# Performance work log

Measured on AMD Instinct MI355X. Metric: run time of the kernel, lower is better.

The kernel has to match this reference:

```python
import jax, jax.numpy as jnp
import numpy as np

D_MODEL = 5120
N_HEADS = 8
D_HEAD = D_MODEL // N_HEADS          # 640
D_ROPE = 16
SPLIT_DIM = D_HEAD - D_ROPE          # 624
D_KV = 128
BATCH, SEQ = 2, 2048
ROPE_SCALE = 40.0


def _rope_cos_sin(seq_len):
    # inv_freq length = D_ROPE//4 (quirk of the original code)
    inv_freq = 1.0 / (10000.0 ** (jnp.arange(0, D_ROPE // 2, 2, dtype=jnp.float32) / (D_ROPE // 2)))
    t = jnp.arange(seq_len, dtype=jnp.float32) / ROPE_SCALE
    freqs = t[:, None] * inv_freq[None, :]            # [S, D_ROPE//4]
    emb = jnp.concatenate([freqs, freqs], axis=-1)    # [S, D_ROPE//2]
    cos = jnp.cos(emb)[None, :, None, :]              # [1,S,1,D_ROPE//2]
    sin = jnp.sin(emb)[None, :, None, :]
    return cos, sin


def _rotate_half(x):
    x1, x2 = jnp.split(x, 2, axis=-1)
    return jnp.concatenate([-x2, x1], axis=-1)


def _apply_rotary(x, cos, sin):
    r = cos.shape[-1]
    x_rot, x_base = x[..., :r], x[..., r:]
    x_rot = x_rot * cos + _rotate_half(x_rot) * sin
    return jnp.concatenate([x_rot, x_base], axis=-1)


def setup_inputs():
    key = jax.random.key(0)
    ks = jax.random.split(key, 18)
    s = 0.02
    inp = {
        'h': jax.random.normal(ks[0], (BATCH, SEQ, D_MODEL), dtype=jnp.float32),
        'W_dkv': jax.random.normal(ks[1], (D_MODEL, D_KV), dtype=jnp.float32) * s,
        'b_dkv': jnp.zeros((D_KV,), jnp.float32),
        'W_dq': jax.random.normal(ks[2], (D_MODEL, D_KV), dtype=jnp.float32) * s,
        'b_dq': jnp.zeros((D_KV,), jnp.float32),
        'W_uk': jax.random.normal(ks[3], (D_KV, N_HEADS * SPLIT_DIM), dtype=jnp.float32) * s,
        'b_uk': jnp.zeros((N_HEADS * SPLIT_DIM,), jnp.float32),
        'W_uv': jax.random.normal(ks[4], (D_KV, N_HEADS * D_HEAD), dtype=jnp.float32) * s,
        'b_uv': jnp.zeros((N_HEADS * D_HEAD,), jnp.float32),
        'W_uq': jax.random.normal(ks[5], (D_KV, N_HEADS * SPLIT_DIM), dtype=jnp.float32) * s,
        'b_uq': jnp.zeros((N_HEADS * SPLIT_DIM,), jnp.float32),
        'W_qr': jax.random.normal(ks[6], (D_KV, N_HEADS * D_ROPE), dtype=jnp.float32) * s,
        'b_qr': jnp.zeros((N_HEADS * D_ROPE,), jnp.float32),
        'W_kr': jax.random.normal(ks[7], (D_MODEL, N_HEADS * D_ROPE), dtype=jnp.float32) * s,
        'b_kr': jnp.zeros((N_HEADS * D_ROPE,), jnp.float32),
        'W_o': jax.random.normal(ks[8], (N_HEADS * D_HEAD, D_MODEL), dtype=jnp.float32) * s,
        'b_o': jnp.zeros((D_MODEL,), jnp.float32),
    }
    return inp


def reference(h, W_dkv, b_dkv, W_dq, b_dq, W_uk, b_uk, W_uv, b_uv,
              W_uq, b_uq, W_qr, b_qr, W_kr, b_kr, W_o, b_o):
    B, S, _ = h.shape
    c_kv = h @ W_dkv + b_dkv                                   # [B,S,D_KV]
    k = (c_kv @ W_uk + b_uk).reshape(B, S, N_HEADS, SPLIT_DIM)
    v = (c_kv @ W_uv + b_uv).reshape(B, S, N_HEADS, D_HEAD)
    c_q = h @ W_dq + b_dq
    q_base = (c_q @ W_uq + b_uq).reshape(B, S, N_HEADS, SPLIT_DIM)
    q_rot = (c_q @ W_qr + b_qr).reshape(B, S, N_HEADS, D_ROPE)
    cos, sin = _rope_cos_sin(S)
    q_rot = _apply_rotary(q_rot, cos, sin)
    k_rot = _apply_rotary((h @ W_kr + b_kr).reshape(B, S, N_HEADS, D_ROPE), cos, sin)
    q = jnp.concatenate([q_base, q_rot], axis=-1)              # [B,S,H,D_HEAD]
    k = jnp.concatenate([k, k_rot], axis=-1)                   # [B,S,H,D_HEAD]
    scores = jnp.einsum('bqhd,bkhd->bhqk', q, k) / jnp.sqrt(jnp.float32(D_HEAD))
    attn = jax.nn.softmax(scores, axis=-1)
    out = jnp.einsum('bhqk,bkhd->bqhd', attn, v)               # [B,S,H,D_HEAD]
    return out.reshape(B, S, N_HEADS * D_HEAD) @ W_o + b_o
```

## Files before the change

### kernel.cpp

```cpp
#include <hip/hip_runtime.h>


typedef unsigned short ushort_t;
typedef __attribute__((ext_vector_type(8)))  short          short8;
typedef __attribute__((ext_vector_type(8)))  unsigned short us8;
typedef __attribute__((ext_vector_type(4)))  float          f32x4;

#define SCALE_ATT 0.0395284707521047f

static __device__ inline unsigned short f2bf(float f) {
  union { float f; unsigned u; } v; v.f = f;
  unsigned r = (v.u + 0x7fffu + ((v.u >> 16) & 1u)) >> 16;
  return (unsigned short)r;
}
static __device__ inline float bf2f(unsigned short u) {
  union { unsigned u; float f; } v; v.u = ((unsigned)u) << 16;
  return v.f;
}
static __device__ inline unsigned cvt_pk_bf16(float a, float b) {
  unsigned r;
  asm("v_cvt_pk_bf16_f32 %0, %1, %2" : "=v"(r) : "v"(a), "v"(b));
  return r;
}
static __device__ inline f32x4 MFMA(short8 a, short8 b, f32x4 c) {
  return __builtin_amdgcn_mfma_f32_16x16x32_bf16(a, b, c, 0, 0, 0);
}

__global__ __launch_bounds__(256) void k_bvec_init(const float* __restrict__ bo,
                                                   float* __restrict__ bvec) {
  int n = blockIdx.x * 256 + threadIdx.x;
  bvec[n] = bo[n];
}

__global__ __launch_bounds__(128) void k_bqabs(const float* __restrict__ buq,
                                               const float* __restrict__ Wuk,
                                               float* __restrict__ bqabs) {
  int h = blockIdx.x, j = threadIdx.x;
  float acc = 0.f;
  const float* bq = buq + h * 624;
  const float* wk = Wuk + (size_t)j * 4992 + h * 624;
  for (int d = 0; d < 624; ++d) acc += bq[d] * wk[d];
  bqabs[h * 128 + j] = acc;
}

__global__ __launch_bounds__(256) void k_wqk(const float* __restrict__ Wuq,
                                             const float* __restrict__ Wuk,
                                             ushort_t* __restrict__ wqkT) {
  __shared__ float Aq[16 * 132];
  __shared__ float Ak[16 * 132];
  int jt = blockIdx.x, it = blockIdx.y, h = blockIdx.z;
  int i0 = it * 16, j0 = jt * 16;
  int t = threadIdx.x;
  int srow = t >> 4, sc0 = (t & 15) * 8;
  int ti = t & 15, tj = t >> 4;
  float acc = 0.f;
  for (int dc = 0; dc < 624; dc += 128) {
#pragma unroll
    for (int i = 0; i < 8; ++i) {
      int d = dc + sc0 + i;
      Aq[srow * 132 + sc0 + i] = (d < 624) ? Wuq[(size_t)(i0 + srow) * 4992 + h * 624 + d] : 0.f;
      Ak[srow * 132 + sc0 + i] = (d < 624) ? Wuk[(size_t)(j0 + srow) * 4992 + h * 624 + d] : 0.f;
    }
    __syncthreads();
    int cs = (624 - dc) < 128 ? (624 - dc) : 128;
    for (int d = 0; d < cs; d += 4) {
      const f32x4 a4 = *(const f32x4*)&Aq[ti * 132 + d];
      const f32x4 b4 = *(const f32x4*)&Ak[tj * 132 + d];
      acc += a4[0] * b4[0] + a4[1] * b4[1] + a4[2] * b4[2] + a4[3] * b4[3];
    }
    __syncthreads();
  }
  wqkT[(size_t)h * 16384 + (size_t)(j0 + tj) * 128 + (i0 + ti)] = f2bf(acc);
}

__global__ __launch_bounds__(256) void k_gemm1_sk(
    const float* __restrict__ H, const float* __restrict__ Wdkv,
    const float* __restrict__ Wdq, const float* __restrict__ Wkr,
    float* __restrict__ part) {
  __shared__ __align__(16) ushort_t As[64 * 72];
  __shared__ __align__(16) ushort_t Bs[192 * 72];
  const int tid = threadIdx.x;
  const int m0 = blockIdx.x * 64;
  const int n0 = blockIdx.y * 192;
  const int kc0 = blockIdx.z * 1280;
  const int lane = tid & 63, wid = tid >> 6;
  const int quad = lane >> 4, l15 = lane & 15;
  f32x4 acc[4][3];
#pragma unroll
  for (int a = 0; a < 4; ++a)
#pragma unroll
    for (int b = 0; b < 3; ++b) acc[a][b] = (f32x4){0.f, 0.f, 0.f, 0.f};
  const int ar = tid >> 2, ak0 = (tid & 3) * 16;
  const int br = tid >> 2, bsg = tid & 3;
  const int bkidx = br ^ (bsg << 4);
  const float* harow = H + (size_t)(m0 + ar) * 5120 + ak0;
  for (int kb = kc0; kb < kc0 + 1280; kb += 64) {
    const float* ap = harow + kb;
    us8 av0, av1;
#pragma unroll
    for (int i = 0; i < 8; ++i) { av0[i] = f2bf(ap[i]); av1[i] = f2bf(ap[8 + i]); }
    *(us8*)&As[ar * 72 + ak0] = av0;
    *(us8*)&As[ar * 72 + ak0 + 8] = av1;
#pragma unroll
    for (int g16 = 0; g16 < 3; ++g16) {
      const int lcol = g16 * 64 + bsg * 16;
      const int col = n0 + lcol;
      const float* base = (col < 128 ? Wdkv + col
                         : col < 256 ? Wdq + (col - 128)
                                     : Wkr + (col - 256)) + (size_t)(kb + br) * 128;
#pragma unroll
      for (int i = 0; i < 16; ++i)
        Bs[(lcol + i) * 72 + bkidx] = f2bf(base[i]);
    }
    __syncthreads();
#pragma unroll
    for (int ks = 0; ks < 2; ++ks) {
      short8 a[4], b[3];
#pragma unroll
      for (int mt = 0; mt < 4; ++mt)
        a[mt] = *(const short8*)&As[(mt * 16 + l15) * 72 + ks * 32 + quad * 8];
#pragma unroll
      for (int nt = 0; nt < 3; ++nt)
        b[nt] = *(const short8*)&Bs[(wid * 48 + nt * 16 + l15) * 72 +
                                    ((ks * 32 + quad * 8) ^ (((wid * 3 + nt) & 3) << 4))];
#pragma unroll
      for (int mt = 0; mt < 4; ++mt)
#pragma unroll
        for (int nt = 0; nt < 3; ++nt) acc[mt][nt] = MFMA(a[mt], b[nt], acc[mt][nt]);
    }
    __syncthreads();
  }
  const size_t pb = (size_t)blockIdx.z * 4096 * 384;
#pragma unroll
  for (int mt = 0; mt < 4; ++mt)
#pragma unroll
    for (int nt = 0; nt < 3; ++nt) {
      const int col = n0 + wid * 48 + nt * 16 + l15;
#pragma unroll
      for (int r = 0; r < 4; ++r) {
        const int row = m0 + mt * 16 + quad * 4 + r;
        part[pb + (size_t)row * 384 + col] = acc[mt][nt][r];
      }
    }
}

__global__ __launch_bounds__(384) void k_reduce(
    const float* __restrict__ part, const float* __restrict__ bdkv,
    const float* __restrict__ bdq, const float* __restrict__ bkr,
    ushort_t* __restrict__ ckv, ushort_t* __restrict__ cq,
    ushort_t* __restrict__ krot) {
  const int row = blockIdx.x;
  const int c = threadIdx.x;
  float v = 0.f;
#pragma unroll
  for (int ks = 0; ks < 4; ++ks)
    v += part[((size_t)ks * 4096 + row) * 384 + c];
  if (c < 128) {
    v += bdkv[c];
    ckv[(size_t)row * 128 + c] = f2bf(v);
  } else if (c < 256) {
    v += bdq[c - 128];
    cq[(size_t)row * 128 + (c - 128)] = f2bf(v);
  } else {
    v += bkr[c - 256];
    float partner = __shfl_xor(v, 4);
    const int j = (c - 256) & 15;
    const int head = (c - 256) >> 4;
    const int s = row & 2047, bb = row >> 11;
    const int j4 = j & 3;
    const float fr = (j4 == 0) ? 1.f : (j4 == 1) ? 0.1f : (j4 == 2) ? 0.01f : 0.001f;
    float sth, cth;
    __sincosf(s * 0.025f * fr, &sth, &cth);
    const float y = (j < 4) ? (v * cth - partner * sth)
                  : (j < 8) ? (v * cth + partner * sth) : v;
    krot[((size_t)((bb << 3) + head) * 2048 + s) * 16 + j] = f2bf(y);
  }
}

__global__ __launch_bounds__(256) void k_ckvt(const ushort_t* __restrict__ ckv,
                                              ushort_t* __restrict__ ckvT) {
  __shared__ __align__(16) ushort_t T[128 * 72];
  const int tid = threadIdx.x;
  const int s0 = blockIdx.x * 64;
  const int bb = s0 >> 11, sl = s0 & 2047;
  const int sr = tid >> 2, sseg = tid & 3;
  {
    const ushort_t* kp = ckv + ((size_t)s0 + sr) * 128 + sseg * 32;
    us8 v[4];
#pragma unroll
    for (int w = 0; w < 4; ++w) v[w] = *(const us8*)(kp + w * 8);
#pragma unroll
    for (int w = 0; w < 4; ++w)
#pragma unroll
      for (int i = 0; i < 8; ++i)
        T[(sseg * 32 + w * 8 + i) * 72 + sr] = v[w][i];
  }
  __syncthreads();
  const int vrow = tid >> 1, vk0 = (tid & 1) * 32;
#pragma unroll
  for (int w = 0; w < 4; ++w) {
    us8 t = *(const us8*)&T[vrow * 72 + vk0 + w * 8];
    *(us8*)(ckvT + ((size_t)bb * 128 + vrow) * 2048 + sl + vk0 + w * 8) = t;
  }
}

__global__ __launch_bounds__(256) void k_qrot(const ushort_t* __restrict__ cq,
                                              const float* __restrict__ Wqr,
                                              const float* __restrict__ bqr,
                                              ushort_t* __restrict__ qrot) {
  int gidx = blockIdx.x * 256 + threadIdx.x;
  int s = gidx & 2047, bh = gidx >> 11;
  int hh = bh & 7, bb = bh >> 3;
  const ushort_t* crow = cq + ((size_t)bb * 2048 + s) * 128;
  float acc[16];
#pragma unroll
  for (int j = 0; j < 16; ++j) acc[j] = bqr[hh * 16 + j];
  for (int k0 = 0; k0 < 128; k0 += 8) {
    us8 cv8 = *(const us8*)(crow + k0);
#pragma unroll
    for (int i = 0; i < 8; ++i) {
      float cv = bf2f(cv8[i]);
      const float* wr = Wqr + (size_t)(k0 + i) * 128 + hh * 16;
#pragma unroll
      for (int j = 0; j < 16; ++j) acc[j] += cv * wr[j];
    }
  }
  float y[16];
#pragma unroll
  for (int j4 = 0; j4 < 4; ++j4) {
    float fr = (j4 == 0) ? 1.f : (j4 == 1) ? 0.1f : (j4 == 2) ? 0.01f : 0.001f;
    float sth, cth;
    __sincosf(s * 0.025f * fr, &sth, &cth);
    y[j4] = acc[j4] * cth - acc[j4 + 4] * sth;
    y[j4 + 4] = acc[j4 + 4] * cth + acc[j4] * sth;
  }
#pragma unroll
  for (int j = 8; j < 16; ++j) y[j] = acc[j];
  us8 o0, o1;
#pragma unroll
  for (int j = 0; j < 8; ++j) {
    o0[j] = f2bf(y[j] * SCALE_ATT);
    o1[j] = f2bf(y[8 + j] * SCALE_ATT);
  }
  *(us8*)(qrot + (size_t)gidx * 16) = o0;
  *(us8*)(qrot + (size_t)gidx * 16 + 8) = o1;
}

__global__ __launch_bounds__(256) void k_qabs(const ushort_t* __restrict__ cq,
                                              const ushort_t* __restrict__ wqkT,
                                              const float* __restrict__ bqabs,
                                              ushort_t* __restrict__ qabs) {
  __shared__ __align__(16) ushort_t As[128 * 72];
  __shared__ __align__(16) ushort_t Bs[128 * 72];
  const int tid = threadIdx.x;
  const int m0 = blockIdx.x * 128, hh = blockIdx.y;
  const int lane = tid & 63, wid = tid >> 6;
  const int quad = lane >> 4, l15 = lane & 15;
  const int wm = wid & 1, wn = wid >> 1;
  f32x4 acc[4][4];
#pragma unroll
  for (int a = 0; a < 4; ++a)
#pragma unroll
    for (int b = 0; b < 4; ++b) acc[a][b] = (f32x4){0.f, 0.f, 0.f, 0.f};
  const int ar = tid >> 1, as0 = (tid & 1) * 32;
  for (int kb = 0; kb < 128; kb += 64) {
    const ushort_t* ap = cq + (size_t)(m0 + ar) * 128 + kb + as0;
    const ushort_t* bp = wqkT + (size_t)hh * 16384 + (size_t)ar * 128 + kb + as0;
#pragma unroll
    for (int w = 0; w < 4; ++w) {
      *(us8*)&As[ar * 72 + as0 + w * 8] = *(const us8*)(ap + w * 8);
      *(us8*)&Bs[ar * 72 + as0 + w * 8] = *(const us8*)(bp + w * 8);
    }
    __syncthreads();
#pragma unroll
    for (int ks = 0; ks < 2; ++ks) {
      short8 a[4], b[4];
#pragma unroll
      for (int mt = 0; mt < 4; ++mt)
        a[mt] = *(const short8*)&As[(wm * 64 + mt * 16 + l15) * 72 + ks * 32 + quad * 8];
#pragma unroll
      for (int nt = 0; nt < 4; ++nt)
        b[nt] = *(const short8*)&Bs[(wn * 64 + nt * 16 + l15) * 72 + ks * 32 + quad * 8];
#pragma unroll
      for (int mt = 0; mt < 4; ++mt)
#pragma unroll
        for (int nt = 0; nt < 4; ++nt) acc[mt][nt] = MFMA(a[mt], b[nt], acc[mt][nt]);
    }
    __syncthreads();
  }
#pragma unroll
  for (int mt = 0; mt < 4; ++mt)
#pragma unroll
    for (int nt = 0; nt < 4; ++nt) {
      int col = wn * 64 + nt * 16 + l15;
      float bias = bqabs[hh * 128 + col];
#pragma unroll
      for (int r = 0; r < 4; ++r) {
        int m = m0 + wm * 64 + mt * 16 + quad * 4 + r;
        int bb = m >> 11, s = m & 2047;
        qabs[((size_t)((bb << 3) + hh) * 2048 + s) * 128 + col] =
            f2bf((acc[mt][nt][r] + bias) * SCALE_ATT);
      }
    }
}

__global__ __launch_bounds__(256) void k_comb(const float* __restrict__ Wo,
                                              const float* __restrict__ Wuv,
                                              const float* __restrict__ buv,
                                              ushort_t* __restrict__ wcombT,
                                              float* __restrict__ bvec) {
  __shared__ __align__(16) ushort_t As[128 * 72];
  __shared__ __align__(16) ushort_t Bs[128 * 72];
  const int tid = threadIdx.x;
  const int n0 = blockIdx.x * 128, hh = blockIdx.y;
  const int lane = tid & 63, wid = tid >> 6;
  const int quad = lane >> 4, l15 = lane & 15;
  const int wm = wid & 1, wn = wid >> 1;
  f32x4 acc[4][4];
#pragma unroll
  for (int a = 0; a < 4; ++a)
#pragma unroll
    for (int b = 0; b < 4; ++b) acc[a][b] = (f32x4){0.f, 0.f, 0.f, 0.f};
  const int ad = tid >> 2, asg = tid & 3;
  const int an0 = asg * 32;
  const int akidx = ad ^ (asg << 4);
  const int bc = tid >> 1, bd0 = (tid & 1) * 32;
  const int bvc = tid >> 1, bvh = tid & 1;
  const int bsgr = (bvc >> 5) & 3;
  const float* buvh = buv + hh * 640;
  float bacc = 0.f;
  for (int kb = 0; kb < 640; kb += 64) {
    const float* ap = Wo + (size_t)(hh * 640 + kb + ad) * 5120 + n0 + an0;
#pragma unroll
    for (int i = 0; i < 32; ++i) As[(an0 + i) * 72 + akidx] = f2bf(ap[i]);
    const float* bp = Wuv + (size_t)bc * 5120 + hh * 640 + kb + bd0;
    us8 bv0, bv1, bv2, bv3;
#pragma unroll
    for (int i = 0; i < 8; ++i) {
      bv0[i] = f2bf(bp[i]); bv1[i] = f2bf(bp[8 + i]);
      bv2[i] = f2bf(bp[16 + i]); bv3[i] = f2bf(bp[24 + i]);
    }
    *(us8*)&Bs[bc * 72 + bd0] = bv0;
    *(us8*)&Bs[bc * 72 + bd0 + 8] = bv1;
    *(us8*)&Bs[bc * 72 + bd0 + 16] = bv2;
    *(us8*)&Bs[bc * 72 + bd0 + 24] = bv3;
    __syncthreads();
#pragma unroll
    for (int d8 = 0; d8 < 4; ++d8) {
      const int k0 = bvh * 32 + d8 * 8;
      const us8 a8 = *(const us8*)&As[bvc * 72 + (k0 ^ (bsgr << 4))];
      const f32x4 b4a = *(const f32x4*)&buvh[kb + k0];
      const f32x4 b4b = *(const f32x4*)&buvh[kb + k0 + 4];
      bacc += b4a[0] * bf2f(a8[0]) + b4a[1] * bf2f(a8[1]) +
              b4a[2] * bf2f(a8[2]) + b4a[3] * bf2f(a8[3]) +
              b4b[0] * bf2f(a8[4]) + b4b[1] * bf2f(a8[5]) +
              b4b[2] * bf2f(a8[6]) + b4b[3] * bf2f(a8[7]);
    }
#pragma unroll
    for (int ks = 0; ks < 2; ++ks) {
      short8 a[4], b[4];
#pragma unroll
      for (int mt = 0; mt < 4; ++mt)
        a[mt] = *(const short8*)&As[(wm * 64 + mt * 16 + l15) * 72 +
                                    ((ks * 32 + quad * 8) ^ (((wm * 2 + (mt >> 1)) & 3) << 4))];
#pragma unroll
      for (int nt = 0; nt < 4; ++nt)
        b[nt] = *(const short8*)&Bs[(wn * 64 + nt * 16 + l15) * 72 + ks * 32 + quad * 8];
#pragma unroll
      for (int mt = 0; mt < 4; ++mt)
#pragma unroll
        for (int nt = 0; nt < 4; ++nt) acc[mt][nt] = MFMA(a[mt], b[nt], acc[mt][nt]);
    }
    __syncthreads();
  }
#pragma unroll
  for (int mt = 0; mt < 4; ++mt)
#pragma unroll
    for (int nt = 0; nt < 4; ++nt) {
      int col = wn * 64 + nt * 16 + l15;
#pragma unroll
      for (int r = 0; r < 4; ++r) {
        int n = n0 + wm * 64 + mt * 16 + quad * 4 + r;
        wcombT[(size_t)n * 1024 + hh * 128 + col] = f2bf(acc[mt][nt][r]);
      }
    }
  atomicAdd(&bvec[n0 + bvc], bacc);
}

__global__ __launch_bounds__(256) void k_attn(const ushort_t* __restrict__ qabs,
                                              const ushort_t* __restrict__ qrot,
                                              const ushort_t* __restrict__ ckv,
                                              const ushort_t* __restrict__ krot,
                                              const ushort_t* __restrict__ ckvT,
                                              ushort_t* __restrict__ ctx) {
  __shared__ __align__(16) ushort_t Qs[64 * 168];
  __shared__ __align__(16) ushort_t Ks[64 * 168];
  __shared__ __align__(16) ushort_t Vt[128 * 72];
  __shared__ __align__(16) ushort_t Ps[64 * 72];
  const int tid = threadIdx.x;
  const int bh = blockIdx.y, bb = bh >> 3, hh = bh & 7;
  const int q0 = blockIdx.x * 64;
  const int lane = tid & 63, wid = tid >> 6;
  const int quad = lane >> 4, l15 = lane & 15;
  const int sr = tid >> 2, sseg = tid & 3;
  const int vrow = tid >> 1, vk0 = (tid & 1) * 32;
  (void)hh;
  {
    const ushort_t* qa = qabs + ((size_t)bh * 2048 + q0 + sr) * 128 + sseg * 32;
#pragma unroll
    for (int w = 0; w < 4; ++w)
      *(us8*)&Qs[sr * 168 + sseg * 32 + w * 8] = *(const us8*)(qa + w * 8);
    if (sseg == 0) {
      const ushort_t* qr = qrot + ((size_t)bh * 2048 + q0 + sr) * 16;
      *(us8*)&Qs[sr * 168 + 128] = *(const us8*)qr;
      *(us8*)&Qs[sr * 168 + 136] = *(const us8*)(qr + 8);
    }
    if (sseg == 1) {
      us8 z = (us8)0;
      *(us8*)&Qs[sr * 168 + 144] = z;
      *(us8*)&Qs[sr * 168 + 152] = z;
      *(us8*)&Ks[sr * 168 + 144] = z;
      *(us8*)&Ks[sr * 168 + 152] = z;
    }
  }
  us8 kreg[4], vreg[4], krr0, krr1;
  auto loadKV = [&](int key0) {
    const ushort_t* kp = ckv + ((size_t)bb * 2048 + key0 + sr) * 128 + sseg * 32;
#pragma unroll
    for (int w = 0; w < 4; ++w) kreg[w] = *(const us8*)(kp + w * 8);
    const ushort_t* vp = ckvT + ((size_t)bb * 128 + vrow) * 2048 + key0 + vk0;
#pragma unroll
    for (int w = 0; w < 4; ++w) vreg[w] = *(const us8*)(vp + w * 8);
    if (sseg == 0) {
      const ushort_t* kr = krot + ((size_t)bh * 2048 + key0 + sr) * 16;
      krr0 = *(const us8*)kr;
      krr1 = *(const us8*)(kr + 8);
    }
  };
  loadKV(0);
  f32x4 oacc[8];
#pragma unroll
  for (int i = 0; i < 8; ++i) oacc[i] = (f32x4){0.f, 0.f, 0.f, 0.f};
  float mrow[4] = {-1e30f, -1e30f, -1e30f, -1e30f};
  float lrow[4] = {0.f, 0.f, 0.f, 0.f};

  for (int kt = 0; kt < 32; ++kt) {
#pragma unroll
    for (int w = 0; w < 4; ++w)
      *(us8*)&Ks[sr * 168 + sseg * 32 + w * 8] = kreg[w];
    if (sseg == 0) {
      *(us8*)&Ks[sr * 168 + 128] = krr0;
      *(us8*)&Ks[sr * 168 + 136] = krr1;
    }
#pragma unroll
    for (int w = 0; w < 4; ++w)
      *(us8*)&Vt[vrow * 72 + vk0 + w * 8] = vreg[w];
    __syncthreads();
    f32x4 sacc[4];
#pragma unroll
    for (int nt = 0; nt < 4; ++nt) sacc[nt] = (f32x4){0.f, 0.f, 0.f, 0.f};
#pragma unroll
    for (int ks = 0; ks < 5; ++ks) {
      short8 aq = *(const short8*)&Qs[(wid * 16 + l15) * 168 + ks * 32 + quad * 8];
#pragma unroll
      for (int nt = 0; nt < 4; ++nt) {
        short8 bk = *(const short8*)&Ks[(nt * 16 + l15) * 168 + ks * 32 + quad * 8];
        sacc[nt] = MFMA(aq, bk, sacc[nt]);
      }
    }
    if (kt < 31) loadKV((kt + 1) * 64);
    float p[4][4];
#pragma unroll
    for (int r = 0; r < 4; ++r) {
      float mx = fmaxf(fmaxf(sacc[0][r], sacc[1][r]), fmaxf(sacc[2][r], sacc[3][r]));
#pragma unroll
      for (int off = 1; off < 16; off <<= 1) mx = fmaxf(mx, __shfl_xor(mx, off));
      if (mx > mrow[r]) {
        float alpha = __expf(mrow[r] - mx);
        mrow[r] = mx;
        lrow[r] *= alpha;
#pragma unroll
        for (int t8 = 0; t8 < 8; ++t8) oacc[t8][r] *= alpha;
      }
      float rs = 0.f;
#pragma unroll
      for (int nt = 0; nt < 4; ++nt) {
        float pv = __expf(sacc[nt][r] - mrow[r]);
        p[nt][r] = pv;
        rs += pv;
      }
      lrow[r] += rs;
    }
#pragma unroll
    for (int nt = 0; nt < 4; ++nt)
#pragma unroll
      for (int rp = 0; rp < 2; ++rp) {
        unsigned pk = cvt_pk_bf16(p[nt][2 * rp], p[nt][2 * rp + 1]);
        int ad = (wid * 16 + quad * 4 + 2 * rp) * 72 + nt * 16 + l15;
        Ps[ad] = (ushort_t)pk;
        Ps[ad + 72] = (ushort_t)(pk >> 16);
      }
    __syncthreads();
#pragma unroll
    for (int kk = 0; kk < 2; ++kk) {
      short8 pa = *(const short8*)&Ps[(wid * 16 + l15) * 72 + kk * 32 + quad * 8];
#pragma unroll
      for (int nt = 0; nt < 8; ++nt) {
        short8 vb = *(const short8*)&Vt[(nt * 16 + l15) * 72 + kk * 32 + quad * 8];
        oacc[nt] = MFMA(pa, vb, oacc[nt]);
      }
    }
    __syncthreads();
  }
#pragma unroll
  for (int r = 0; r < 4; ++r) {
#pragma unroll
    for (int off = 1; off < 16; off <<= 1) lrow[r] += __shfl_xor(lrow[r], off);
    float rl = 1.f / lrow[r];
    int row = q0 + wid * 16 + quad * 4 + r;
    size_t base = ((size_t)bb * 2048 + row) * 1024 + hh * 128;
#pragma unroll
    for (int nt = 0; nt < 8; ++nt)
      ctx[base + nt * 16 + l15] = f2bf(oacc[nt][r] * rl);
  }
}

__global__ __launch_bounds__(256) void k_final(const ushort_t* __restrict__ ctx,
                                               const ushort_t* __restrict__ wcombT,
                                               const float* __restrict__ bvec,
                                               float* __restrict__ out) {
  __shared__ __align__(16) ushort_t As[128 * 72];
  __shared__ __align__(16) ushort_t Bs[128 * 72];
  const int tid = threadIdx.x;
  const int m0 = blockIdx.x * 128, n0 = blockIdx.y * 128;
  const int lane = tid & 63, wid = tid >> 6;
  const int quad = lane >> 4, l15 = lane & 15;
  const int wm = wid & 1, wn = wid >> 1;
  f32x4 acc[4][4];
#pragma unroll
  for (int a = 0; a < 4; ++a)
#pragma unroll
    for (int b = 0; b < 4; ++b) acc[a][b] = (f32x4){0.f, 0.f, 0.f, 0.f};
  const int ar = tid >> 1, as0 = (tid & 1) * 32;
  const ushort_t* ap = ctx + (size_t)(m0 + ar) * 1024 + as0;
  const ushort_t* bp = wcombT + (size_t)(n0 + ar) * 1024 + as0;
  us8 ra[4], rb[4];
#pragma unroll
  for (int w = 0; w < 4; ++w) {
    ra[w] = *(const us8*)(ap + w * 8);
    rb[w] = *(const us8*)(bp + w * 8);
  }
  for (int kb = 0; kb < 1024; kb += 64) {
#pragma unroll
    for (int w = 0; w < 4; ++w) {
      *(us8*)&As[ar * 72 + as0 + w * 8] = ra[w];
      *(us8*)&Bs[ar * 72 + as0 + w * 8] = rb[w];
    }
    __syncthreads();
    if (kb < 960) {
      const ushort_t* ap2 = ap + kb + 64;
      const ushort_t* bp2 = bp + kb + 64;
#pragma unroll
      for (int w = 0; w < 4; ++w) {
        ra[w] = *(const us8*)(ap2 + w * 8);
        rb[w] = *(const us8*)(bp2 + w * 8);
      }
    }
#pragma unroll
    for (int ks = 0; ks < 2; ++ks) {
      short8 a[4], b[4];
#pragma unroll
      for (int mt = 0; mt < 4; ++mt)
        a[mt] = *(const short8*)&As[(wm * 64 + mt * 16 + l15) * 72 + ks * 32 + quad * 8];
#pragma unroll
      for (int nt = 0; nt < 4; ++nt)
        b[nt] = *(const short8*)&Bs[(wn * 64 + nt * 16 + l15) * 72 + ks * 32 + quad * 8];
#pragma unroll
      for (int mt = 0; mt < 4; ++mt)
#pragma unroll
        for (int nt = 0; nt < 4; ++nt) acc[mt][nt] = MFMA(a[mt], b[nt], acc[mt][nt]);
    }
    __syncthreads();
  }
#pragma unroll
  for (int mt = 0; mt < 4; ++mt)
#pragma unroll
    for (int nt = 0; nt < 4; ++nt) {
      int col = wn * 64 + nt * 16 + l15;
      float bias = bvec[n0 + col];
#pragma unroll
      for (int r = 0; r < 4; ++r) {
        int row = m0 + wm * 64 + mt * 16 + quad * 4 + r;
        out[(size_t)row * 5120 + n0 + col] = acc[mt][nt][r] + bias;
      }
    }
}

extern "C" void kernel_launch(void* const* d_in, const int* in_sizes, int n_in,
                              void* d_out, int out_size, void* d_ws, size_t ws_size,
                              hipStream_t stream) {
  const float* H    = (const float*)d_in[0];
  const float* Wdkv = (const float*)d_in[1];
  const float* bdkv = (const float*)d_in[2];
  const float* Wdq  = (const float*)d_in[3];
  const float* bdq  = (const float*)d_in[4];
  const float* Wuk  = (const float*)d_in[5];
  const float* Wuv  = (const float*)d_in[7];
  const float* buv  = (const float*)d_in[8];
  const float* Wuq  = (const float*)d_in[9];
  const float* buq  = (const float*)d_in[10];
  const float* Wqr  = (const float*)d_in[11];
  const float* bqr  = (const float*)d_in[12];
  const float* Wkr  = (const float*)d_in[13];
  const float* bkr  = (const float*)d_in[14];
  const float* Wo   = (const float*)d_in[15];
  const float* bo   = (const float*)d_in[16];
  float* out = (float*)d_out;

  char* ws = (char*)d_ws;
  size_t off = 0;
  auto alloc = [&](size_t bytes) -> void* {
    void* p = ws + off;
    off += (bytes + 255) & ~(size_t)255;
    return p;
  };
  ushort_t* ckv    = (ushort_t*)alloc((size_t)4096 * 128 * 2);
  ushort_t* cq     = (ushort_t*)alloc((size_t)4096 * 128 * 2);
  ushort_t* ckvT   = (ushort_t*)alloc((size_t)2 * 128 * 2048 * 2);
  ushort_t* krot   = (ushort_t*)alloc((size_t)16 * 2048 * 16 * 2);
  ushort_t* qrot   = (ushort_t*)alloc((size_t)16 * 2048 * 16 * 2);
  ushort_t* wqkT   = (ushort_t*)alloc((size_t)8 * 128 * 128 * 2);
  float*    bqabs  = (float*)alloc((size_t)8 * 128 * 4);
  float*    bvec   = (float*)alloc((size_t)5120 * 4);
  size_t mark = off;
  float*    part   = (float*)alloc((size_t)4 * 4096 * 384 * 4);
  size_t endB = off;
  off = mark;
  ushort_t* qabs   = (ushort_t*)alloc((size_t)16 * 2048 * 128 * 2);
  ushort_t* wcombT = (ushort_t*)alloc((size_t)5120 * 1024 * 2);
  ushort_t* ctx    = (ushort_t*)alloc((size_t)4096 * 1024 * 2);
  if (off < endB) off = endB;
  (void)ws_size; (void)in_sizes; (void)n_in; (void)out_size;

  hipLaunchKernelGGL(k_bvec_init, dim3(20), dim3(256), 0, stream, bo, bvec);
  hipLaunchKernelGGL(k_bqabs, dim3(8), dim3(128), 0, stream, buq, Wuk, bqabs);
  hipLaunchKernelGGL(k_wqk, dim3(8, 8, 8), dim3(256), 0, stream, Wuq, Wuk, wqkT);
  hipLaunchKernelGGL(k_gemm1_sk, dim3(64, 2, 4), dim3(256), 0, stream,
                     H, Wdkv, Wdq, Wkr, part);
  hipLaunchKernelGGL(k_reduce, dim3(4096), dim3(384), 0, stream,
                     part, bdkv, bdq, bkr, ckv, cq, krot);
  hipLaunchKernelGGL(k_ckvt, dim3(64), dim3(256), 0, stream, ckv, ckvT);
  hipLaunchKernelGGL(k_comb, dim3(40, 8), dim3(256), 0, stream, Wo, Wuv, buv, wcombT, bvec);
  hipLaunchKernelGGL(k_qrot, dim3(128), dim3(256), 0, stream, cq, Wqr, bqr, qrot);
  hipLaunchKernelGGL(k_qabs, dim3(32, 8), dim3(256), 0, stream, cq, wqkT, bqabs, qabs);
  hipLaunchKernelGGL(k_attn, dim3(32, 16), dim3(256), 0, stream,
                     qabs, qrot, ckv, krot, ckvT, ctx);
  hipLaunchKernelGGL(k_final, dim3(32, 40), dim3(256), 0, stream, ctx, wcombT, bvec, out);
}
```

Baseline: 679.7 us.

## Transpose attention score tile, vectorize fp32-to-bf16 staging loads in GEMMs

In attention, the score MFMA operands are swapped so each lane holds one query row. The row max then needs only two cross-quad shuffles, the row sum is kept per lane, and P is written to LDS as packed dwords. Because each wave reads back only its own P rows, the barrier between the P write and the PV MFMA is dropped. The first-stage GEMM and the weight-combine kernel now load fp32 with 16-byte vector loads and convert pairs with v_cvt_pk_bf16, using a new XOR swizzle on transposed LDS tiles. The aim is fewer scalar global loads, fewer scalar LDS stores and less softmax shuffle traffic. The risk is more complex row-max bookkeeping, including a wave-level __any branch and per-row rescales fetched by shuffle.

```diff
diff --git a/kernel.cpp b/kernel.cpp
--- a/kernel.cpp
+++ b/kernel.cpp
@@ -5,6 +5,7 @@
 typedef __attribute__((ext_vector_type(8)))  short          short8;
 typedef __attribute__((ext_vector_type(8)))  unsigned short us8;
 typedef __attribute__((ext_vector_type(4)))  float          f32x4;
+typedef __attribute__((ext_vector_type(4)))  unsigned int   u32x4;
 
 #define SCALE_ATT 0.0395284707521047f
 
@@ -91,26 +92,35 @@
 #pragma unroll
     for (int b = 0; b < 3; ++b) acc[a][b] = (f32x4){0.f, 0.f, 0.f, 0.f};
   const int ar = tid >> 2, ak0 = (tid & 3) * 16;
-  const int br = tid >> 2, bsg = tid & 3;
-  const int bkidx = br ^ (bsg << 4);
+  const int bkp = tid >> 3;
+  const int bng = tid & 7;
   const float* harow = H + (size_t)(m0 + ar) * 5120 + ak0;
   for (int kb = kc0; kb < kc0 + 1280; kb += 64) {
     const float* ap = harow + kb;
-    us8 av0, av1;
-#pragma unroll
-    for (int i = 0; i < 8; ++i) { av0[i] = f2bf(ap[i]); av1[i] = f2bf(ap[8 + i]); }
-    *(us8*)&As[ar * 72 + ak0] = av0;
-    *(us8*)&As[ar * 72 + ak0 + 8] = av1;
-#pragma unroll
-    for (int g16 = 0; g16 < 3; ++g16) {
-      const int lcol = g16 * 64 + bsg * 16;
+    f32x4 af0 = *(const f32x4*)ap, af1 = *(const f32x4*)(ap + 4);
+    f32x4 af2 = *(const f32x4*)(ap + 8), af3 = *(const f32x4*)(ap + 12);
+    u32x4 apk0 = { cvt_pk_bf16(af0[0], af0[1]), cvt_pk_bf16(af0[2], af0[3]),
+                   cvt_pk_bf16(af1[0], af1[1]), cvt_pk_bf16(af1[2], af1[3]) };
+    u32x4 apk1 = { cvt_pk_bf16(af2[0], af2[1]), cvt_pk_bf16(af2[2], af2[3]),
+                   cvt_pk_bf16(af3[0], af3[1]), cvt_pk_bf16(af3[2], af3[3]) };
+    *(u32x4*)&As[ar * 72 + ak0] = apk0;
+    *(u32x4*)&As[ar * 72 + ak0 + 8] = apk1;
+    const int krow = kb + 2 * bkp;
+    const int kd = (2 * bkp) ^ (bng << 3);
+#pragma unroll
+    for (int g = 0; g < 3; ++g) {
+      const int lcol = g * 64 + bng * 8;
       const int col = n0 + lcol;
       const float* base = (col < 128 ? Wdkv + col
                          : col < 256 ? Wdq + (col - 128)
-                                     : Wkr + (col - 256)) + (size_t)(kb + br) * 128;
-#pragma unroll
-      for (int i = 0; i < 16; ++i)
-        Bs[(lcol + i) * 72 + bkidx] = f2bf(base[i]);
+                                     : Wkr + (col - 256)) + (size_t)krow * 128;
+      f32x4 r0a = *(const f32x4*)base, r0b = *(const f32x4*)(base + 4);
+      f32x4 r1a = *(const f32x4*)(base + 128), r1b = *(const f32x4*)(base + 132);
+#pragma unroll
+      for (int i = 0; i < 4; ++i) {
+        *(unsigned*)&Bs[(lcol + i) * 72 + kd]     = cvt_pk_bf16(r0a[i], r1a[i]);
+        *(unsigned*)&Bs[(lcol + 4 + i) * 72 + kd] = cvt_pk_bf16(r0b[i], r1b[i]);
+      }
     }
     __syncthreads();
 #pragma unroll
@@ -120,9 +130,11 @@
       for (int mt = 0; mt < 4; ++mt)
         a[mt] = *(const short8*)&As[(mt * 16 + l15) * 72 + ks * 32 + quad * 8];
 #pragma unroll
-      for (int nt = 0; nt < 3; ++nt)
-        b[nt] = *(const short8*)&Bs[(wid * 48 + nt * 16 + l15) * 72 +
-                                    ((ks * 32 + quad * 8) ^ (((wid * 3 + nt) & 3) << 4))];
+      for (int nt = 0; nt < 3; ++nt) {
+        const int row = wid * 48 + nt * 16 + l15;
+        const int kofs = (ks * 32 + quad * 8) ^ (((row >> 3) & 7) << 3);
+        b[nt] = *(const short8*)&Bs[row * 72 + kofs];
+      }
 #pragma unroll
       for (int mt = 0; mt < 4; ++mt)
 #pragma unroll
@@ -321,34 +333,60 @@
   for (int a = 0; a < 4; ++a)
 #pragma unroll
     for (int b = 0; b < 4; ++b) acc[a][b] = (f32x4){0.f, 0.f, 0.f, 0.f};
-  const int ad = tid >> 2, asg = tid & 3;
-  const int an0 = asg * 32;
-  const int akidx = ad ^ (asg << 4);
+  const int akp = tid >> 3;
+  const int ang = tid & 7;
+  const int kd0 = (2 * akp) ^ (((2 * ang) & 7) << 3);
+  const int kd1 = (2 * akp) ^ (((2 * ang + 1) & 7) << 3);
   const int bc = tid >> 1, bd0 = (tid & 1) * 32;
   const int bvc = tid >> 1, bvh = tid & 1;
-  const int bsgr = (bvc >> 5) & 3;
+  const int bswz = ((bvc >> 3) & 7) << 3;
   const float* buvh = buv + hh * 640;
   float bacc = 0.f;
   for (int kb = 0; kb < 640; kb += 64) {
-    const float* ap = Wo + (size_t)(hh * 640 + kb + ad) * 5120 + n0 + an0;
-#pragma unroll
-    for (int i = 0; i < 32; ++i) As[(an0 + i) * 72 + akidx] = f2bf(ap[i]);
+    {
+      const float* ap0 = Wo + (size_t)(hh * 640 + kb + 2 * akp) * 5120 + n0 + ang * 16;
+      const float* ap1 = ap0 + 5120;
+      f32x4 r0[4], r1[4];
+#pragma unroll
+      for (int w = 0; w < 4; ++w) {
+        r0[w] = *(const f32x4*)(ap0 + w * 4);
+        r1[w] = *(const f32x4*)(ap1 + w * 4);
+      }
+#pragma unroll
+      for (int w = 0; w < 2; ++w)
+#pragma unroll
+        for (int i = 0; i < 4; ++i)
+          *(unsigned*)&As[(ang * 16 + w * 4 + i) * 72 + kd0] =
+              cvt_pk_bf16(r0[w][i], r1[w][i]);
+#pragma unroll
+      for (int w = 2; w < 4; ++w)
+#pragma unroll
+        for (int i = 0; i < 4; ++i)
+          *(unsigned*)&As[(ang * 16 + w * 4 + i) * 72 + kd1] =
+              cvt_pk_bf16(r0[w][i], r1[w][i]);
+    }
     const float* bp = Wuv + (size_t)bc * 5120 + hh * 640 + kb + bd0;
-    us8 bv0, bv1, bv2, bv3;
-#pragma unroll
-    for (int i = 0; i < 8; ++i) {
-      bv0[i] = f2bf(bp[i]); bv1[i] = f2bf(bp[8 + i]);
-      bv2[i] = f2bf(bp[16 + i]); bv3[i] = f2bf(bp[24 + i]);
-    }
-    *(us8*)&Bs[bc * 72 + bd0] = bv0;
-    *(us8*)&Bs[bc * 72 + bd0 + 8] = bv1;
-    *(us8*)&Bs[bc * 72 + bd0 + 16] = bv2;
-    *(us8*)&Bs[bc * 72 + bd0 + 24] = bv3;
+    f32x4 b0 = *(const f32x4*)bp, b1 = *(const f32x4*)(bp + 4);
+    f32x4 b2 = *(const f32x4*)(bp + 8), b3 = *(const f32x4*)(bp + 12);
+    f32x4 b4 = *(const f32x4*)(bp + 16), b5 = *(const f32x4*)(bp + 20);
+    f32x4 b6 = *(const f32x4*)(bp + 24), b7 = *(const f32x4*)(bp + 28);
+    u32x4 q0 = { cvt_pk_bf16(b0[0], b0[1]), cvt_pk_bf16(b0[2], b0[3]),
+                 cvt_pk_bf16(b1[0], b1[1]), cvt_pk_bf16(b1[2], b1[3]) };
+    u32x4 q1 = { cvt_pk_bf16(b2[0], b2[1]), cvt_pk_bf16(b2[2], b2[3]),
+                 cvt_pk_bf16(b3[0], b3[1]), cvt_pk_bf16(b3[2], b3[3]) };
+    u32x4 q2 = { cvt_pk_bf16(b4[0], b4[1]), cvt_pk_bf16(b4[2], b4[3]),
+                 cvt_pk_bf16(b5[0], b5[1]), cvt_pk_bf16(b5[2], b5[3]) };
+    u32x4 q3 = { cvt_pk_bf16(b6[0], b6[1]), cvt_pk_bf16(b6[2], b6[3]),
+                 cvt_pk_bf16(b7[0], b7[1]), cvt_pk_bf16(b7[2], b7[3]) };
+    *(u32x4*)&Bs[bc * 72 + bd0]      = q0;
+    *(u32x4*)&Bs[bc * 72 + bd0 + 8]  = q1;
+    *(u32x4*)&Bs[bc * 72 + bd0 + 16] = q2;
+    *(u32x4*)&Bs[bc * 72 + bd0 + 24] = q3;
     __syncthreads();
 #pragma unroll
     for (int d8 = 0; d8 < 4; ++d8) {
       const int k0 = bvh * 32 + d8 * 8;
-      const us8 a8 = *(const us8*)&As[bvc * 72 + (k0 ^ (bsgr << 4))];
+      const us8 a8 = *(const us8*)&As[bvc * 72 + (k0 ^ bswz)];
       const f32x4 b4a = *(const f32x4*)&buvh[kb + k0];
       const f32x4 b4b = *(const f32x4*)&buvh[kb + k0 + 4];
       bacc += b4a[0] * bf2f(a8[0]) + b4a[1] * bf2f(a8[1]) +
@@ -360,9 +398,11 @@
     for (int ks = 0; ks < 2; ++ks) {
       short8 a[4], b[4];
 #pragma unroll
-      for (int mt = 0; mt < 4; ++mt)
-        a[mt] = *(const short8*)&As[(wm * 64 + mt * 16 + l15) * 72 +
-                                    ((ks * 32 + quad * 8) ^ (((wm * 2 + (mt >> 1)) & 3) << 4))];
+      for (int mt = 0; mt < 4; ++mt) {
+        const int row = wm * 64 + mt * 16 + l15;
+        const int kofs = (ks * 32 + quad * 8) ^ (((row >> 3) & 7) << 3);
+        a[mt] = *(const short8*)&As[row * 72 + kofs];
+      }
 #pragma unroll
       for (int nt = 0; nt < 4; ++nt)
         b[nt] = *(const short8*)&Bs[(wn * 64 + nt * 16 + l15) * 72 + ks * 32 + quad * 8];
@@ -442,7 +482,8 @@
 #pragma unroll
   for (int i = 0; i < 8; ++i) oacc[i] = (f32x4){0.f, 0.f, 0.f, 0.f};
   float mrow[4] = {-1e30f, -1e30f, -1e30f, -1e30f};
-  float lrow[4] = {0.f, 0.f, 0.f, 0.f};
+  float m_sm = -1e30f;
+  float lrow_l = 0.f;
 
   for (int kt = 0; kt < 32; ++kt) {
 #pragma unroll
@@ -465,42 +506,44 @@
 #pragma unroll
       for (int nt = 0; nt < 4; ++nt) {
         short8 bk = *(const short8*)&Ks[(nt * 16 + l15) * 168 + ks * 32 + quad * 8];
-        sacc[nt] = MFMA(aq, bk, sacc[nt]);
+        sacc[nt] = MFMA(bk, aq, sacc[nt]);
       }
     }
     if (kt < 31) loadKV((kt + 1) * 64);
-    float p[4][4];
-#pragma unroll
-    for (int r = 0; r < 4; ++r) {
-      float mx = fmaxf(fmaxf(sacc[0][r], sacc[1][r]), fmaxf(sacc[2][r], sacc[3][r]));
-#pragma unroll
-      for (int off = 1; off < 16; off <<= 1) mx = fmaxf(mx, __shfl_xor(mx, off));
-      if (mx > mrow[r]) {
-        float alpha = __expf(mrow[r] - mx);
-        mrow[r] = mx;
-        lrow[r] *= alpha;
-#pragma unroll
-        for (int t8 = 0; t8 < 8; ++t8) oacc[t8][r] *= alpha;
-      }
-      float rs = 0.f;
-#pragma unroll
-      for (int nt = 0; nt < 4; ++nt) {
-        float pv = __expf(sacc[nt][r] - mrow[r]);
-        p[nt][r] = pv;
-        rs += pv;
-      }
-      lrow[r] += rs;
-    }
+    float mx = sacc[0][0];
 #pragma unroll
     for (int nt = 0; nt < 4; ++nt)
 #pragma unroll
-      for (int rp = 0; rp < 2; ++rp) {
-        unsigned pk = cvt_pk_bf16(p[nt][2 * rp], p[nt][2 * rp + 1]);
-        int ad = (wid * 16 + quad * 4 + 2 * rp) * 72 + nt * 16 + l15;
-        Ps[ad] = (ushort_t)pk;
-        Ps[ad + 72] = (ushort_t)(pk >> 16);
-      }
-    __syncthreads();
+      for (int r = 0; r < 4; ++r) mx = fmaxf(mx, sacc[nt][r]);
+    mx = fmaxf(mx, __shfl_xor(mx, 16));
+    mx = fmaxf(mx, __shfl_xor(mx, 32));
+    const bool grew = mx > m_sm;
+    if (__any(grew)) {
+      if (grew) { lrow_l *= __expf(m_sm - mx); m_sm = mx; }
+#pragma unroll
+      for (int r = 0; r < 4; ++r) {
+        float mnew = __shfl(m_sm, quad * 4 + r);
+        if (mnew > mrow[r]) {
+          float alpha = __expf(mrow[r] - mnew);
+          mrow[r] = mnew;
+#pragma unroll
+          for (int t8 = 0; t8 < 8; ++t8) oacc[t8][r] *= alpha;
+        }
+      }
+    }
+    float rs = 0.f;
+    const int prow = (wid * 16 + l15) * 72 + quad * 4;
+#pragma unroll
+    for (int nt = 0; nt < 4; ++nt) {
+      float p0 = __expf(sacc[nt][0] - m_sm);
+      float p1 = __expf(sacc[nt][1] - m_sm);
+      float p2 = __expf(sacc[nt][2] - m_sm);
+      float p3 = __expf(sacc[nt][3] - m_sm);
+      rs += (p0 + p1) + (p2 + p3);
+      *(unsigned*)&Ps[prow + nt * 16]     = cvt_pk_bf16(p0, p1);
+      *(unsigned*)&Ps[prow + nt * 16 + 2] = cvt_pk_bf16(p2, p3);
+    }
+    lrow_l += rs;
 #pragma unroll
     for (int kk = 0; kk < 2; ++kk) {
       short8 pa = *(const short8*)&Ps[(wid * 16 + l15) * 72 + kk * 32 + quad * 8];
@@ -512,11 +555,11 @@
     }
     __syncthreads();
   }
+  lrow_l += __shfl_xor(lrow_l, 16);
+  lrow_l += __shfl_xor(lrow_l, 32);
 #pragma unroll
   for (int r = 0; r < 4; ++r) {
-#pragma unroll
-    for (int off = 1; off < 16; off <<= 1) lrow[r] += __shfl_xor(lrow[r], off);
-    float rl = 1.f / lrow[r];
+    float rl = 1.f / __shfl(lrow_l, quad * 4 + r);
     int row = q0 + wid * 16 + quad * 4 + r;
     size_t base = ((size_t)bb * 2048 + row) * 1024 + hh * 128;
 #pragma unroll
```

After: 652.6 us. 1.04x faster.
